# Optimization experiments

Hardware: AMD Instinct MI355X
Metric: run time of the kernel (lower is better)

The kernel has to match this reference:

```python
import jax, jax.numpy as jnp
from jax import lax
import numpy as np

GRID_SIZE = 5   # spline_points
DEGREE = 3      # spline_degree
NUM_BASES = GRID_SIZE + DEGREE  # 8 basis functions per input element


def make_grid():
    # efficient-kan style uniform grid on [-1, 1] extended by DEGREE knots each side
    h = 2.0 / GRID_SIZE
    return jnp.arange(-DEGREE, GRID_SIZE + DEGREE + 1, dtype=jnp.float32) * h - 1.0  # [G+2k+1]


def b_splines(x, grid, k):
    """Cox-de Boor B-spline bases. x: [N, F] -> [N, F, G+k]."""
    x = x[..., None]  # [N, F, 1]
    bases = ((x >= grid[:-1]) & (x < grid[1:])).astype(x.dtype)  # order 0
    for d in range(1, k + 1):
        left = (x - grid[:-(d + 1)]) / (grid[d:-1] - grid[:-(d + 1)])
        right = (grid[d + 1:] - x) / (grid[d + 1:] - grid[1:-d])
        bases = left * bases[..., :-1] + right * bases[..., 1:]
    return bases


def kan_conv(x, base_w, spline_w, ksize, pad, grid):
    """KANConv2d: unfold patches, apply KANLinear (silu base + spline term).
    x: [B, C, H, W]; base_w: [O, C*k*k]; spline_w: [O, C*k*k, NUM_BASES]."""
    patches = lax.conv_general_dilated_patches(
        x, (ksize, ksize), (1, 1), [(pad, pad), (pad, pad)])  # [B, C*k*k, Ho, Wo]
    B, F, Ho, Wo = patches.shape
    p = patches.transpose(0, 2, 3, 1).reshape(-1, F)  # [B*Ho*Wo, F]
    base = jax.nn.silu(p) @ base_w.T
    bs = b_splines(p, grid, DEGREE).reshape(p.shape[0], F * NUM_BASES)
    sp = bs @ spline_w.reshape(spline_w.shape[0], F * NUM_BASES).T
    out = base + sp  # [B*Ho*Wo, O]
    return out.reshape(B, Ho, Wo, -1).transpose(0, 3, 1, 2)


def maxpool2(x):
    return lax.reduce_window(x, -jnp.inf, lax.max, (1, 1, 2, 2), (1, 1, 2, 2), 'VALID')


def setup_inputs() -> dict:
    key = jax.random.key(0)
    ks = jax.random.split(key, 12)
    def w(k, shape, fan_in):
        return jax.random.normal(k, shape, dtype=jnp.float32) / np.sqrt(fan_in)
    B = 2048
    return {
        'x': jax.random.normal(ks[0], (B, 1, 28, 28), dtype=jnp.float32),
        'base_w1': w(ks[1], (4, 1 * 9), 9),
        'spline_w1': w(ks[2], (4, 1 * 9, NUM_BASES), 9 * NUM_BASES) * 0.1,
        'base_w2': w(ks[3], (8, 4 * 9), 36),
        'spline_w2': w(ks[4], (8, 4 * 9, NUM_BASES), 36 * NUM_BASES) * 0.1,
        'base_w3': w(ks[5], (16, 8 * 9), 72),
        'spline_w3': w(ks[6], (16, 8 * 9, NUM_BASES), 72 * NUM_BASES) * 0.1,
        'base_w4': w(ks[7], (32, 16 * 4), 64),
        'spline_w4': w(ks[8], (32, 16 * 4, NUM_BASES), 64 * NUM_BASES) * 0.1,
        'fc_w': w(ks[9], (10, 32), 32),
        'fc_b': jnp.zeros((10,), dtype=jnp.float32),
    }


def reference(x, base_w1, spline_w1, base_w2, spline_w2, base_w3, spline_w3,
              base_w4, spline_w4, fc_w, fc_b):
    grid = make_grid()
    h = kan_conv(x, base_w1, spline_w1, 3, 1, grid)   # [B,4,28,28]
    h = maxpool2(h)                                   # [B,4,14,14]
    h = kan_conv(h, base_w2, spline_w2, 3, 1, grid)   # [B,8,14,14]
    h = maxpool2(h)                                   # [B,8,7,7]
    h = kan_conv(h, base_w3, spline_w3, 3, 1, grid)   # [B,16,7,7]
    h = maxpool2(h)                                   # [B,16,3,3]
    h = kan_conv(h, base_w4, spline_w4, 2, 1, grid)   # [B,32,4,4]
    h = jnp.mean(h, axis=(2, 3))                      # global avg pool -> [B,32]
    return h @ fc_w.T + fc_b                          # [B,10]
```

## Files before the change

kernel.cpp:

```cpp
#include <hip/hip_runtime.h>

#define DEV __device__ __forceinline__

typedef __fp16 h8 __attribute__((ext_vector_type(8)));
typedef __fp16 f2 __attribute__((ext_vector_type(2)));
typedef float f32x4 __attribute__((ext_vector_type(4)));
union U4H { uint4 u; h8 h; };
union HS { _Float16 h; unsigned short s; };

DEV unsigned h16(float x) { HS z; z.h = (_Float16)x; return (unsigned)z.s; }
DEV unsigned f2bits(f2 h) { union { f2 h; unsigned u; } x; x.h = h; return x.u; }
DEV float silu_f(float v) { return v / (1.0f + __expf(-v)); }

#define SIL_OFF 16448

DEV void bspline8(float x, float bb[8]) {
    float b[11];
#pragma unroll
    for (int i = 0; i < 11; ++i) {
        float g0 = (i - 3) * 0.4f - 1.0f;
        float g1 = (i - 2) * 0.4f - 1.0f;
        b[i] = ((x >= g0) && (x < g1)) ? 1.0f : 0.0f;
    }
#pragma unroll
    for (int d = 1; d <= 3; ++d) {
        const float inv = 1.0f / (0.4f * (float)d);
#pragma unroll
        for (int i = 0; i < 11 - d; ++i) {
            float gl = (i - 3) * 0.4f - 1.0f;
            float gr = (i - 3 + d + 1) * 0.4f - 1.0f;
            b[i] = (x - gl) * inv * b[i] + (gr - x) * inv * b[i + 1];
        }
    }
#pragma unroll
    for (int j = 0; j < 8; ++j) bb[j] = b[j];
}

DEV unsigned silpair(float sil) {
    unsigned sh = h16(sil);
    float shf = (float)(_Float16)sil;
    unsigned slo = h16(sil - shf);
    return sh | (slo << 16);
}

template <int CIN, int H, int W>
DEV void expand(const float* src, char* planes, int tid) {
    constexpr int WC = W + 2, HC = H + 2;
    constexpr int CELLS = CIN * HC * WC;
    const int ln = tid & 63;
    for (int cell = tid; cell < CELLS; cell += 256) {
        int c = cell / (HC * WC);
        int rr = cell - c * (HC * WC);
        int row = rr / WC, col = rr - row * WC;
        int y = row - 1, x = col - 1;
        bool yin = (unsigned)y < (unsigned)H;
        const float* srow = src + c * H * W + y * W;

        float v0 = (yin && (unsigned)x < (unsigned)W) ? srow[x] : 0.0f;

        float u = (v0 + 2.2f) * 2.5f;
        int mi = (int)u;
        bool valid = (u >= 0.0f) && (u < 11.0f);
        float t = u - (float)mi;
        float t2 = t * t, t3 = t2 * t;
        float omt = 1.0f - t;
        float p3 = omt * omt * omt * (1.0f / 6.0f);
        float p2 = (3.0f * t3 - 6.0f * t2 + 4.0f) * (1.0f / 6.0f);
        float p1 = (-3.0f * t3 + 3.0f * t2 + 3.0f * t + 1.0f) * (1.0f / 6.0f);
        float p0 = t3 * (1.0f / 6.0f);
        unsigned d0 = f2bits(__builtin_amdgcn_cvt_pkrtz(p3, p2));
        unsigned d1 = f2bits(__builtin_amdgcn_cvt_pkrtz(p1, p0));
        unsigned long long P = ((unsigned long long)d1 << 32) | d0;
        unsigned long long lo64 = 0ull, hi64 = 0ull;
        int shamt = (mi - 3) * 16;
        if (valid) {
            if (shamt < 0) {
                lo64 = P >> (-shamt);
            } else if (shamt < 64) {
                lo64 = P << shamt;
                hi64 = shamt ? (P >> (64 - shamt)) : 0ull;
            } else {
                hi64 = P << (shamt - 64);
            }
        }
        uint4 brec;
        brec.x = (unsigned)lo64;
        brec.y = (unsigned)(lo64 >> 32);
        brec.z = (unsigned)hi64;
        brec.w = (unsigned)(hi64 >> 32);

        unsigned sp0 = silpair(silu_f(v0));
        unsigned sp1 = __shfl_down(sp0, 1);
        unsigned sp2 = __shfl_down(sp0, 2);
        if (ln >= 62) {
            float v1 = (yin && (unsigned)(x + 1) < (unsigned)W) ? srow[x + 1] : 0.0f;
            float v2 = (yin && (unsigned)(x + 2) < (unsigned)W) ? srow[x + 2] : 0.0f;
            sp1 = silpair(silu_f(v1));
            sp2 = silpair(silu_f(v2));
        }
        uint4 srec;
        srec.x = sp0;
        srec.y = sp1;
        srec.z = sp2;
        srec.w = 0u;

        *(uint4*)(planes + (size_t)cell * 16) = brec;
        *(uint4*)(planes + SIL_OFF + (size_t)cell * 16) = srec;
    }
}

template <int HC, int SC>
DEV constexpr int chunkcell(int rc) {
    return ((rc / 3) * HC + (rc % 3)) * SC;
}

template <int O, int PHV, int PWV>
DEV void poolwrite(f32x4 acc, int ty, int tx, int ln, float* s_next) {
    const int n = ln & 15, q = ln >> 4;
    float q0 = fmaxf(acc[0], acc[1]);
    float q1 = fmaxf(acc[2], acc[3]);
    float r0 = fmaxf(q0, __shfl_xor(q0, 32));
    float r1 = fmaxf(q1, __shfl_xor(q1, 32));
    if (ln < 32 && n < O && ty < PHV) {
        int ppx = tx * 4 + (q & 1) * 2;
        float* dst = s_next + n * (PHV * PWV) + ty * PWV + ppx;
        if (ppx < PWV) dst[0] = r0;
        if (ppx + 1 < PWV) dst[1] = r1;
    }
}

template <int CIN, int H, int W, int O, int KC, int BWC, int TX, int TPW,
          int PHV, int PWV>
DEV void layer_mfma(const uint4* __restrict__ pwB, const char* planes,
                    float* s_next, int tid) {
    constexpr int HC = H + 2, SC = W + 2;
    const int wv = tid >> 6, ln = tid & 63;
    const int m = ln & 15;
    const int half = ln >> 4;
    const int lane_off = (half == 3) ? SIL_OFF : half * 16;

    if constexpr (KC == BWC) {
        uint4 bw[BWC];
#pragma unroll
        for (int i = 0; i < BWC; ++i) bw[i] = pwB[i * 64 + ln];
#pragma unroll
        for (int tt = 0; tt < TPW; ++tt) {
            const int gid = wv * TPW + tt;
            const int ty = gid / TX, tx = gid - ty * TX;
            const int py = min(2 * ty + (m >> 3), H - 1);
            const int px = min(tx * 8 + (m & 7), W - 1);
            const int base = (py * SC + px) * 16 + lane_off;
            f32x4 acc = {0.f, 0.f, 0.f, 0.f};
#pragma unroll
            for (int i = 0; i < BWC; ++i) {
                const int off = chunkcell<HC, SC>(i) * 16;
                U4H a; a.u = *(const uint4*)(planes + base + off);
                U4H b; b.u = bw[i];
                acc = __builtin_amdgcn_mfma_f32_16x16x32_f16(a.h, b.h, acc, 0, 0, 0);
            }
            poolwrite<O, PHV, PWV>(acc, ty, tx, ln, s_next);
        }
    } else {
        f32x4 acc[TPW];
        int base[TPW], tyA[TPW], txA[TPW];
#pragma unroll
        for (int tt = 0; tt < TPW; ++tt) {
            acc[tt] = {0.f, 0.f, 0.f, 0.f};
            const int gid = wv * TPW + tt;
            tyA[tt] = gid / TX;
            txA[tt] = gid - tyA[tt] * TX;
            const int py = min(2 * tyA[tt] + (m >> 3), H - 1);
            const int px = min(txA[tt] * 8 + (m & 7), W - 1);
            base[tt] = (py * SC + px) * 16 + lane_off;
        }
#pragma unroll
        for (int kc = 0; kc < KC; kc += BWC) {
            uint4 bw[BWC];
#pragma unroll
            for (int i = 0; i < BWC; ++i) bw[i] = pwB[(kc + i) * 64 + ln];
#pragma unroll
            for (int i = 0; i < BWC; ++i) {
                const int off = chunkcell<HC, SC>(kc + i) * 16;
#pragma unroll
                for (int tt = 0; tt < TPW; ++tt) {
                    U4H a; a.u = *(const uint4*)(planes + base[tt] + off);
                    U4H b; b.u = bw[i];
                    acc[tt] = __builtin_amdgcn_mfma_f32_16x16x32_f16(a.h, b.h, acc[tt], 0, 0, 0);
                }
            }
        }
#pragma unroll
        for (int tt = 0; tt < TPW; ++tt)
            poolwrite<O, PHV, PWV>(acc[tt], tyA[tt], txA[tt], ln, s_next);
    }
}

DEV float wval(const float* wb, const float* ws, int NT, int O, int n, int k) {
    int chunk = k >> 5, s = k & 31;
    int cin = chunk / 3, dy = chunk - 3 * (chunk / 3);
    if (n >= O) return 0.f;
    if (s < 24) {
        int dx = s >> 3, j = s & 7;
        return ws[(n * NT + cin * 9 + dy * 3 + dx) * 8 + j];
    }
    if (s < 30) {
        int dx = (s - 24) >> 1;
        return (float)(_Float16)wb[n * NT + cin * 9 + dy * 3 + dx];
    }
    return 0.f;
}

DEV unsigned packw(float a, float b) { return h16(a) | (h16(b) << 16); }

__global__ __launch_bounds__(256) void kan_prep(
    const float* __restrict__ wb1, const float* __restrict__ ws1,
    const float* __restrict__ wb2, const float* __restrict__ ws2,
    const float* __restrict__ wb3, const float* __restrict__ ws3,
    const float* __restrict__ wb4, const float* __restrict__ ws4,
    float* __restrict__ wsbase) {
    float* wr = wsbase;
    const int bid = blockIdx.x;
    const int tid = threadIdx.x;

    if (bid == 0) {
        for (int i = tid; i < 512; i += 256) {
            int o = i / 16, c = i % 16;
            float s = 0.0f;
#pragma unroll
            for (int q = 0; q < 4; ++q) s += wb4[o * 64 + c * 4 + q];
            wr[i] = s;
        }
    } else if (bid == 1) {
        __shared__ float zb[8];
        if (tid == 0) {
            float zbb[8];
            bspline8(0.0f, zbb);
#pragma unroll
            for (int j = 0; j < 8; ++j) zb[j] = zbb[j];
        }
        __syncthreads();
        const int o = tid >> 3, j = tid & 7;
        float s = 0.0f;
        for (int f = 0; f < 64; ++f) s += ws4[(o * 64 + f) * 8 + j];
        s *= zb[j];
        s += __shfl_xor(s, 1);
        s += __shfl_xor(s, 2);
        s += __shfl_xor(s, 4);
        if (j == 0) wr[4608 + o] = 7.0f * s;
    } else if (bid < 18) {
        const int i = (bid - 2) * 256 + tid;
        int j = i % 8, c = (i / 8) % 16, o = i / 128;
        float s = 0.0f;
#pragma unroll
        for (int q = 0; q < 4; ++q) s += ws4[(o * 64 + c * 4 + q) * 8 + j];
        wr[512 + i] = s;
    } else {
        int g = (bid - 18) * 256 + tid;
        if (g < 9984) {
            const float *wb, *ws;
            unsigned* dst;
            int NT, O, rel;
            if (g < 768) {
                wb = wb1; ws = ws1; NT = 9; O = 4; rel = g;
                dst = (unsigned*)(wsbase + 4640);
            } else if (g < 3840) {
                wb = wb2; ws = ws2; NT = 36; O = 8; rel = g - 768;
                dst = (unsigned*)(wsbase + 5408);
            } else {
                wb = wb3; ws = ws3; NT = 72; O = 16; rel = g - 3840;
                dst = (unsigned*)(wsbase + 8480);
            }
            int kf = rel >> 8;
            int lane = (rel >> 2) & 63;
            int j = rel & 3;
            int k0 = kf * 32 + ((lane >> 4) & 3) * 8 + j * 2;
            int n = lane & 15;
            dst[rel] = packw(wval(wb, ws, NT, O, n, k0),
                             wval(wb, ws, NT, O, n, k0 + 1));
        }
    }
}

__global__ __launch_bounds__(256, 4) void kan_fused(
    const float* __restrict__ x, const float* __restrict__ wsbase,
    const float* __restrict__ fcw, const float* __restrict__ fcb,
    float* __restrict__ out) {
    __shared__ uint4 s_planes4[2052];
    __shared__ float s_next[784];
    __shared__ float s_sum[144];
    __shared__ float s_pool[32];
    char* planes = (char*)s_planes4;

    const int b = blockIdx.x;
    const int tid = threadIdx.x;
    const float* wr = wsbase;
    const uint4* pw1 = (const uint4*)(wsbase + 4640);
    const uint4* pw2 = (const uint4*)(wsbase + 5408);
    const uint4* pw3 = (const uint4*)(wsbase + 8480);

    expand<1, 28, 28>(x + (size_t)b * 784, planes, tid);
    __syncthreads();
    layer_mfma<1, 28, 28, 4, 3, 3, 4, 14, 14, 14>(pw1, planes, s_next, tid);
    __syncthreads();

    expand<4, 14, 14>(s_next, planes, tid);
    __syncthreads();
    layer_mfma<4, 14, 14, 8, 12, 6, 2, 4, 7, 7>(pw2, planes, s_next, tid);
    __syncthreads();

    expand<8, 7, 7>(s_next, planes, tid);
    __syncthreads();
    layer_mfma<8, 7, 7, 16, 24, 8, 1, 1, 3, 3>(pw3, planes, s_next, tid);
    __syncthreads();

    float* s_exp = (float*)s_planes4;
    if (tid < 144) {
        float v = s_next[tid];
        float bb[8];
        bspline8(v, bb);
        s_exp[tid * 9 + 0] = silu_f(v);
#pragma unroll
        for (int j = 0; j < 8; ++j) s_exp[tid * 9 + 1 + j] = bb[j];
    }
    __syncthreads();
    if (tid < 144) {
        int c = tid / 9, comp = tid - (tid / 9) * 9;
        float s = 0.0f;
#pragma unroll
        for (int p = 0; p < 9; ++p) s += s_exp[(c * 9 + p) * 9 + comp];
        s_sum[tid] = s;
    }
    __syncthreads();
    if (tid < 32) {
        int o = tid;
        float acc = wr[4608 + o];
        for (int c = 0; c < 16; ++c) {
            acc += wr[o * 16 + c] * s_sum[c * 9 + 0];
#pragma unroll
            for (int j = 0; j < 8; ++j)
                acc += wr[512 + (o * 16 + c) * 8 + j] * s_sum[c * 9 + 1 + j];
        }
        s_pool[o] = acc * (1.0f / 16.0f);
    }
    __syncthreads();
    if (tid < 10) {
        float acc = fcb[tid];
#pragma unroll
        for (int c = 0; c < 32; ++c) acc += fcw[tid * 32 + c] * s_pool[c];
        out[(size_t)b * 10 + tid] = acc;
    }
}

extern "C" void kernel_launch(void* const* d_in, const int* in_sizes, int n_in,
                              void* d_out, int out_size, void* d_ws, size_t ws_size,
                              hipStream_t stream) {
    const float* x = (const float*)d_in[0];
    const float* wb1 = (const float*)d_in[1];
    const float* ws1 = (const float*)d_in[2];
    const float* wb2 = (const float*)d_in[3];
    const float* ws2 = (const float*)d_in[4];
    const float* wb3 = (const float*)d_in[5];
    const float* ws3 = (const float*)d_in[6];
    const float* wb4 = (const float*)d_in[7];
    const float* ws4 = (const float*)d_in[8];
    const float* fcw = (const float*)d_in[9];
    const float* fcb = (const float*)d_in[10];
    float* out = (float*)d_out;

    const int B = in_sizes[0] / (28 * 28);
    float* wsbase = (float*)d_ws;

    kan_prep<<<57, 256, 0, stream>>>(wb1, ws1, wb2, ws2, wb3, ws3, wb4, ws4,
                                     wsbase);
    kan_fused<<<B, 256, 0, stream>>>(x, wsbase, fcw, fcb, out);
}
```

Baseline: 51.83 us.

## Halve shared plane buffer via windowed expansion to double block occupancy

Shrinks the shared expanded-plane buffer to about half its size by processing each layer in two windows: layer 1 in two row halves, and layers 2 and 3 in two channel halves whose MFMA results accumulate across passes. Scratch arrays are aliased into the plane buffer, and launch bounds are raised so eight 256-thread blocks can be resident per CU. This trades extra barriers and duplicated halo expansion for more concurrent blocks to hide latency. Register pressure under the tighter launch bound may cause spills.

```diff
diff --git a/kernel.cpp b/kernel.cpp
--- a/kernel.cpp
+++ b/kernel.cpp
@@ -12,7 +12,7 @@
 DEV unsigned f2bits(f2 h) { union { f2 h; unsigned u; } x; x.h = h; return x.u; }
 DEV float silu_f(float v) { return v / (1.0f + __expf(-v)); }
 
-#define SIL_OFF 16448
+#define SIL_OFF 8256
 
 DEV void bspline8(float x, float bb[8]) {
     float b[11];
@@ -43,16 +43,16 @@
     return sh | (slo << 16);
 }
 
-template <int CIN, int H, int W>
-DEV void expand(const float* src, char* planes, int tid) {
-    constexpr int WC = W + 2, HC = H + 2;
-    constexpr int CELLS = CIN * HC * WC;
+template <int CINP, int H, int W, int NROWS>
+DEV void expand_win(const float* src, int row0, char* planes, int tid) {
+    constexpr int WC = W + 2;
+    constexpr int CELLS = CINP * NROWS * WC;
     const int ln = tid & 63;
     for (int cell = tid; cell < CELLS; cell += 256) {
-        int c = cell / (HC * WC);
-        int rr = cell - c * (HC * WC);
-        int row = rr / WC, col = rr - row * WC;
-        int y = row - 1, x = col - 1;
+        int c = cell / (NROWS * WC);
+        int rr = cell - c * (NROWS * WC);
+        int r = rr / WC, col = rr - r * WC;
+        int y = row0 + r - 1, x = col - 1;
         bool yin = (unsigned)y < (unsigned)H;
         const float* srow = src + c * H * W + y * W;
 
@@ -109,9 +109,9 @@
     }
 }
 
-template <int HC, int SC>
+template <int NROWS, int SC>
 DEV constexpr int chunkcell(int rc) {
-    return ((rc / 3) * HC + (rc % 3)) * SC;
+    return ((rc / 3) * NROWS + (rc % 3)) * SC;
 }
 
 template <int O, int PHV, int PWV>
@@ -129,69 +129,82 @@
     }
 }
 
-template <int CIN, int H, int W, int O, int KC, int BWC, int TX, int TPW,
-          int PHV, int PWV>
-DEV void layer_mfma(const uint4* __restrict__ pwB, const char* planes,
-                    float* s_next, int tid) {
-    constexpr int HC = H + 2, SC = W + 2;
+template <int H, int W, int O, int KC, int TX, int TPW, int PHV, int PWV,
+          int NROWS>
+DEV void conv_pool_l1(const uint4* __restrict__ pwB, const char* planes,
+                      float* s_next, int tid, int ty_off) {
+    constexpr int SC = W + 2;
     const int wv = tid >> 6, ln = tid & 63;
     const int m = ln & 15;
     const int half = ln >> 4;
     const int lane_off = (half == 3) ? SIL_OFF : half * 16;
 
-    if constexpr (KC == BWC) {
+    uint4 bw[KC];
+#pragma unroll
+    for (int i = 0; i < KC; ++i) bw[i] = pwB[i * 64 + ln];
+#pragma unroll
+    for (int tt = 0; tt < TPW; ++tt) {
+        const int gid = wv * TPW + tt;
+        const int tyl = gid / TX, tx = gid - tyl * TX;
+        const int py = 2 * tyl + (m >> 3);
+        const int px = min(tx * 8 + (m & 7), W - 1);
+        const int base = (py * SC + px) * 16 + lane_off;
+        f32x4 acc = {0.f, 0.f, 0.f, 0.f};
+#pragma unroll
+        for (int i = 0; i < KC; ++i) {
+            const int off = chunkcell<NROWS, SC>(i) * 16;
+            U4H a; a.u = *(const uint4*)(planes + base + off);
+            U4H b; b.u = bw[i];
+            acc = __builtin_amdgcn_mfma_f32_16x16x32_f16(a.h, b.h, acc, 0, 0, 0);
+        }
+        poolwrite<O, PHV, PWV>(acc, ty_off + tyl, tx, ln, s_next);
+    }
+}
+
+template <int H, int W, int KCP, int BWC, int TX, int TPW, int NROWS>
+DEV void conv_accum(const uint4* __restrict__ pwB, const char* planes, int tid,
+                    f32x4* acc) {
+    constexpr int SC = W + 2;
+    const int wv = tid >> 6, ln = tid & 63;
+    const int m = ln & 15;
+    const int half = ln >> 4;
+    const int lane_off = (half == 3) ? SIL_OFF : half * 16;
+
+    int base[TPW];
+#pragma unroll
+    for (int tt = 0; tt < TPW; ++tt) {
+        const int gid = wv * TPW + tt;
+        const int ty = gid / TX, tx = gid - ty * TX;
+        const int py = min(2 * ty + (m >> 3), H - 1);
+        const int px = min(tx * 8 + (m & 7), W - 1);
+        base[tt] = (py * SC + px) * 16 + lane_off;
+    }
+#pragma unroll
+    for (int kc = 0; kc < KCP; kc += BWC) {
         uint4 bw[BWC];
 #pragma unroll
-        for (int i = 0; i < BWC; ++i) bw[i] = pwB[i * 64 + ln];
-#pragma unroll
-        for (int tt = 0; tt < TPW; ++tt) {
-            const int gid = wv * TPW + tt;
-            const int ty = gid / TX, tx = gid - ty * TX;
-            const int py = min(2 * ty + (m >> 3), H - 1);
-            const int px = min(tx * 8 + (m & 7), W - 1);
-            const int base = (py * SC + px) * 16 + lane_off;
-            f32x4 acc = {0.f, 0.f, 0.f, 0.f};
-#pragma unroll
-            for (int i = 0; i < BWC; ++i) {
-                const int off = chunkcell<HC, SC>(i) * 16;
-                U4H a; a.u = *(const uint4*)(planes + base + off);
+        for (int i = 0; i < BWC; ++i) bw[i] = pwB[(kc + i) * 64 + ln];
+#pragma unroll
+        for (int i = 0; i < BWC; ++i) {
+            const int off = chunkcell<NROWS, SC>(kc + i) * 16;
+#pragma unroll
+            for (int tt = 0; tt < TPW; ++tt) {
+                U4H a; a.u = *(const uint4*)(planes + base[tt] + off);
                 U4H b; b.u = bw[i];
-                acc = __builtin_amdgcn_mfma_f32_16x16x32_f16(a.h, b.h, acc, 0, 0, 0);
+                acc[tt] = __builtin_amdgcn_mfma_f32_16x16x32_f16(a.h, b.h, acc[tt], 0, 0, 0);
             }
-            poolwrite<O, PHV, PWV>(acc, ty, tx, ln, s_next);
-        }
-    } else {
-        f32x4 acc[TPW];
-        int base[TPW], tyA[TPW], txA[TPW];
-#pragma unroll
-        for (int tt = 0; tt < TPW; ++tt) {
-            acc[tt] = {0.f, 0.f, 0.f, 0.f};
-            const int gid = wv * TPW + tt;
-            tyA[tt] = gid / TX;
-            txA[tt] = gid - tyA[tt] * TX;
-            const int py = min(2 * tyA[tt] + (m >> 3), H - 1);
-            const int px = min(txA[tt] * 8 + (m & 7), W - 1);
-            base[tt] = (py * SC + px) * 16 + lane_off;
-        }
-#pragma unroll
-        for (int kc = 0; kc < KC; kc += BWC) {
-            uint4 bw[BWC];
-#pragma unroll
-            for (int i = 0; i < BWC; ++i) bw[i] = pwB[(kc + i) * 64 + ln];
-#pragma unroll
-            for (int i = 0; i < BWC; ++i) {
-                const int off = chunkcell<HC, SC>(kc + i) * 16;
-#pragma unroll
-                for (int tt = 0; tt < TPW; ++tt) {
-                    U4H a; a.u = *(const uint4*)(planes + base[tt] + off);
-                    U4H b; b.u = bw[i];
-                    acc[tt] = __builtin_amdgcn_mfma_f32_16x16x32_f16(a.h, b.h, acc[tt], 0, 0, 0);
-                }
-            }
-        }
-#pragma unroll
-        for (int tt = 0; tt < TPW; ++tt)
-            poolwrite<O, PHV, PWV>(acc[tt], tyA[tt], txA[tt], ln, s_next);
+        }
+    }
+}
+
+template <int O, int TX, int TPW, int PHV, int PWV>
+DEV void pool_tiles(const f32x4* acc, int tid, float* s_next) {
+    const int wv = tid >> 6, ln = tid & 63;
+#pragma unroll
+    for (int tt = 0; tt < TPW; ++tt) {
+        const int gid = wv * TPW + tt;
+        const int ty = gid / TX, tx = gid - ty * TX;
+        poolwrite<O, PHV, PWV>(acc[tt], ty, tx, ln, s_next);
     }
 }
 
@@ -281,14 +294,12 @@
     }
 }
 
-__global__ __launch_bounds__(256, 4) void kan_fused(
+__global__ __launch_bounds__(256, 8) void kan_fused(
     const float* __restrict__ x, const float* __restrict__ wsbase,
     const float* __restrict__ fcw, const float* __restrict__ fcb,
     float* __restrict__ out) {
-    __shared__ uint4 s_planes4[2052];
+    __shared__ uint4 s_planes4[1028];
     __shared__ float s_next[784];
-    __shared__ float s_sum[144];
-    __shared__ float s_pool[32];
     char* planes = (char*)s_planes4;
 
     const int b = blockIdx.x;
@@ -298,22 +309,47 @@
     const uint4* pw2 = (const uint4*)(wsbase + 5408);
     const uint4* pw3 = (const uint4*)(wsbase + 8480);
 
-    expand<1, 28, 28>(x + (size_t)b * 784, planes, tid);
-    __syncthreads();
-    layer_mfma<1, 28, 28, 4, 3, 3, 4, 14, 14, 14>(pw1, planes, s_next, tid);
-    __syncthreads();
-
-    expand<4, 14, 14>(s_next, planes, tid);
-    __syncthreads();
-    layer_mfma<4, 14, 14, 8, 12, 6, 2, 4, 7, 7>(pw2, planes, s_next, tid);
-    __syncthreads();
-
-    expand<8, 7, 7>(s_next, planes, tid);
-    __syncthreads();
-    layer_mfma<8, 7, 7, 16, 24, 8, 1, 1, 3, 3>(pw3, planes, s_next, tid);
-    __syncthreads();
+#pragma unroll 1
+    for (int p = 0; p < 2; ++p) {
+        expand_win<1, 28, 28, 16>(x + (size_t)b * 784, p * 14, planes, tid);
+        __syncthreads();
+        conv_pool_l1<28, 28, 4, 3, 4, 7, 14, 14, 16>(pw1, planes, s_next, tid,
+                                                     p * 7);
+        __syncthreads();
+    }
+
+    {
+        f32x4 acc[4];
+#pragma unroll
+        for (int i = 0; i < 4; ++i) acc[i] = {0.f, 0.f, 0.f, 0.f};
+#pragma unroll 1
+        for (int p = 0; p < 2; ++p) {
+            expand_win<2, 14, 14, 16>(s_next + p * 392, 0, planes, tid);
+            __syncthreads();
+            conv_accum<14, 14, 6, 6, 2, 4, 16>(pw2 + p * 6 * 64, planes, tid, acc);
+            __syncthreads();
+        }
+        pool_tiles<8, 2, 4, 7, 7>(acc, tid, s_next);
+        __syncthreads();
+    }
+
+    {
+        f32x4 acc1 = {0.f, 0.f, 0.f, 0.f};
+#pragma unroll 1
+        for (int p = 0; p < 2; ++p) {
+            expand_win<4, 7, 7, 9>(s_next + p * 196, 0, planes, tid);
+            __syncthreads();
+            conv_accum<7, 7, 12, 6, 1, 1, 9>(pw3 + p * 12 * 64, planes, tid,
+                                             &acc1);
+            __syncthreads();
+        }
+        pool_tiles<16, 1, 1, 3, 3>(&acc1, tid, s_next);
+        __syncthreads();
+    }
 
     float* s_exp = (float*)s_planes4;
+    float* s_sum = (float*)s_planes4 + 1344;
+    float* s_pool = (float*)s_planes4 + 1504;
     if (tid < 144) {
         float v = s_next[tid];
         float bb[8];
```

New measurement: 48.11 us. 1.08x faster.
